# Optimization experiments

Measured on AMD Instinct MI355X. Metric: run time of the kernel, lower is better.

## Reference

```python
import jax, jax.numpy as jnp
import numpy as np

B, S, NODE, DEP, R, L, E = 32, 1024, 256, 64, 50, 16, 128


def setup_inputs() -> dict:
    key = jax.random.key(0)
    k1, k2, k3, k4, k5 = jax.random.split(key, 5)
    context = jax.random.normal(k1, (B, S, NODE), dtype=jnp.float32)
    # torch.rand -> uniform [0,1); one [dep, node+dep] matrix per dependency relation
    dep_W = jax.random.uniform(k2, (R, DEP, NODE + DEP), dtype=jnp.float32)
    heads = jax.random.randint(k3, (B, L, E), 0, S, dtype=jnp.int32)
    tails = jax.random.randint(k4, (B, L, E), 0, S, dtype=jnp.int32)
    rels = jax.random.randint(k5, (B, L, E), 0, R, dtype=jnp.int32)
    return {"context": context, "dep_W": dep_W, "heads": heads, "tails": tails, "rels": rels}


def reference(context, dep_W, heads, tails, rels):
    # context: [B,S,node]; dep_W: [R,dep,node+dep]; heads/tails/rels: [B,L,E]
    B_, S_, node = context.shape
    dep = dep_W.shape[1]
    E_ = heads.shape[2]
    batch_off = jnp.arange(B_, dtype=jnp.int32)[:, None] * S_  # [B,1]

    def layer_step(child, layer):
        h, t, r = layer  # each [B,E]
        # gather per-edge tail features (node feature ++ child state from deeper layers)
        ctx_t = jnp.take_along_axis(context, t[:, :, None], axis=1)  # [B,E,node]
        chd_t = jnp.take_along_axis(child, t[:, :, None], axis=1)    # [B,E,dep]
        feat = jnp.concatenate([ctx_t, chd_t], axis=-1)              # [B,E,node+dep]
        W_e = dep_W[r]                                               # [B,E,dep,node+dep]
        # sum(W * feat, dim=1) == relation-indexed matvec
        msg = jnp.einsum('bekd,bed->bek', W_e, feat)                 # [B,E,dep]
        # scatter-average messages onto head nodes (per batch -> flat index)
        idx = (batch_off + h).reshape(-1)                            # [B*E]
        seg = jax.ops.segment_sum(msg.reshape(-1, dep), idx, num_segments=B_ * S_)
        cnt = jax.ops.segment_sum(jnp.ones((B_ * E_,), msg.dtype), idx, num_segments=B_ * S_)
        avg = seg / jnp.maximum(cnt, 1.0)[:, None]
        child_flat = child.reshape(B_ * S_, dep)
        # heads touched this layer get the averaged message (assignment semantics)
        child_new = jnp.where((cnt > 0)[:, None], avg, child_flat).reshape(B_, S_, dep)
        return child_new, None

    child0 = jnp.zeros((B_, S_, dep), context.dtype)
    layers = (jnp.moveaxis(heads, 1, 0), jnp.moveaxis(tails, 1, 0), jnp.moveaxis(rels, 1, 0))
    child, _ = jax.lax.scan(layer_step, child0, layers)  # layer 0 = deepest layer
    return jnp.concatenate([context, child], axis=-1)    # [B,S,node+dep]
```

## Files before the change

kernel.cpp:

```cpp
#include <hip/hip_runtime.h>

constexpr int B_ = 32;
constexpr int S_ = 1024;
constexpr int NODE_ = 256;
constexpr int DEP_ = 64;
constexpr int R_ = 50;
constexpr int L_ = 16;
constexpr int E_ = 128;
constexpr int FEAT_ = NODE_ + DEP_;
constexpr int NEDGE_ = B_ * E_;
constexpr int BS_ = B_ * S_;
constexpr int CH_ = 16;
constexpr int NCH_ = 320;
constexpr int PREB_ = 512;

constexpr size_t N_CHILD  = (size_t)BS_ * DEP_;
constexpr size_t OFF_A0   = N_CHILD;
constexpr size_t OFF_WT   = N_CHILD * 4;
constexpr size_t N_WT     = (size_t)R_ * FEAT_ * DEP_;
constexpr size_t OFF_SORT = OFF_WT + N_WT;
constexpr size_t N_SORT   = (size_t)L_ * NEDGE_;
constexpr size_t OFF_CHUNK= OFF_SORT + N_SORT;
constexpr size_t N_CHUNK_I= (size_t)L_ * NCH_ * 4;
constexpr size_t OFF_HC   = OFF_CHUNK + N_CHUNK_I;
constexpr size_t N_HC     = (size_t)L_ * BS_;
constexpr size_t OFF_MT   = OFF_HC + N_HC;
constexpr size_t OFF_MH   = OFF_MT + N_SORT;
constexpr size_t OFF_MI   = OFF_MH + N_SORT;
constexpr size_t OFF_CD   = OFF_MI + N_SORT;
constexpr size_t N_CD     = (size_t)L_ * NEDGE_ * DEP_;

__global__ void k_pre(const float* __restrict__ W, const int* __restrict__ rels,
                      const int* __restrict__ heads,
                      float* __restrict__ WT2, int* __restrict__ sorted,
                      int4* __restrict__ chunks, int* __restrict__ hc,
                      float* __restrict__ zero_base) {
  int blk = blockIdx.x, tid = threadIdx.x;
  if (blk < L_) {
    int l = blk;
    __shared__ int hist[R_], startA[R_], rank[R_], cstart[R_];
    __shared__ int ntot;
    if (tid < R_) { hist[tid] = 0; rank[tid] = 0; }
    int* hcl = hc + (size_t)l * BS_;
    for (int i = tid; i < BS_; i += 256) hcl[i] = 0;
    __syncthreads();
    for (int ed = tid; ed < NEDGE_; ed += 256) {
      int b = ed >> 7, e = ed & (E_ - 1);
      atomicAdd(&hist[rels[(b * L_ + l) * E_ + e]], 1);
      atomicAdd(&hcl[b * S_ + heads[(b * L_ + l) * E_ + e]], 1);
    }
    __syncthreads();
    if (tid == 0) {
      int s = 0, cs = 0;
      for (int r = 0; r < R_; ++r) {
        startA[r] = s; s += hist[r];
        cstart[r] = cs; cs += (hist[r] + CH_ - 1) / CH_;
      }
      ntot = cs;
    }
    __syncthreads();
    for (int ed = tid; ed < NEDGE_; ed += 256) {
      int b = ed >> 7, e = ed & (E_ - 1);
      int r = rels[(b * L_ + l) * E_ + e];
      int pos = startA[r] + atomicAdd(&rank[r], 1);
      sorted[l * NEDGE_ + pos] = ed;
    }
    if (tid < R_) {
      int n = hist[tid], st = startA[tid], cs = cstart[tid];
      for (int m = 0; m * CH_ < n; ++m) {
        int c = n - m * CH_; if (c > CH_) c = CH_;
        chunks[l * NCH_ + cs + m] = make_int4(tid, st + m * CH_, c, 0);
      }
    }
    __syncthreads();
    for (int i = ntot + tid; i < NCH_; i += 256)
      chunks[l * NCH_ + i] = make_int4(0, 0, 0, 0);
  } else {
    int gtid = (blk - L_) * 256 + tid;
    const int NT = PREB_ * 256;
    for (int gid = gtid; gid < (int)N_WT; gid += NT) {
      int r = gid / 20480;
      int rem = gid - r * 20480;
      int i4 = rem >> 8;
      int k = (rem >> 2) & 63;
      int c = rem & 3;
      WT2[gid] = W[((size_t)r * DEP_ + k) * FEAT_ + 4 * i4 + c];
    }
    float4* z4 = (float4*)zero_base;
    int nz4 = (int)((N_CHILD * 2) / 4);
    for (int i = gtid; i < nz4; i += NT) z4[i] = make_float4(0.f, 0.f, 0.f, 0.f);
  }
}

__device__ __forceinline__ float dot64(const float4* __restrict__ f4,
                                       const float4* __restrict__ w) {
  float a0 = 0.f, a1 = 0.f, a2 = 0.f, a3 = 0.f;
#pragma unroll
  for (int i = 0; i < 16; ++i) {
    float4 f = f4[i];
    a0 = fmaf(w[i].x, f.x, a0);
    a1 = fmaf(w[i].y, f.y, a1);
    a2 = fmaf(w[i].z, f.z, a2);
    a3 = fmaf(w[i].w, f.w, a3);
  }
  return (a0 + a1) + (a2 + a3);
}

__global__ void __launch_bounds__(256) k_ctx(
    const float* __restrict__ context, const float* __restrict__ WT2,
    const int* __restrict__ heads, const int* __restrict__ tails,
    const int* __restrict__ sorted, const int4* __restrict__ chunks,
    const int* __restrict__ hc, float* __restrict__ ctxdot,
    int* __restrict__ m_trow, int* __restrict__ m_hrow,
    float* __restrict__ m_invc) {
  int cid = blockIdx.x;
  int l = cid / NCH_;
  int4 ck = chunks[cid];
  int r = ck.x, start = ck.y, ccnt = ck.z;
  if (ccnt == 0) return;
  int tid = threadIdx.x, s = tid >> 6, k = tid & 63;

  __shared__ float feat[CH_][NODE_];
  __shared__ float part[4][CH_][DEP_];
  __shared__ int trows[CH_];
  __shared__ float invs[CH_];

  if (tid < ccnt) {
    int pos = l * NEDGE_ + start + tid;
    int ed = sorted[pos];
    int b = ed >> 7, e = ed & (E_ - 1);
    int t = tails[(b * L_ + l) * E_ + e];
    int h = heads[(b * L_ + l) * E_ + e];
    int trow = b * S_ + t, hrow = b * S_ + h;
    int tch = (l > 0) && (hc[(size_t)(l - 1) * BS_ + trow] > 0);
    float invc = 1.0f / (float)hc[(size_t)l * BS_ + hrow];
    m_trow[pos] = trow | (tch ? (int)0x80000000 : 0);
    m_hrow[pos] = hrow;
    m_invc[pos] = invc;
    trows[tid] = trow;
    invs[tid] = invc;
  }
  __syncthreads();

  int tr[CH_];
#pragma unroll
  for (int j = 0; j < CH_; ++j) tr[j] = trows[(j < ccnt) ? j : (ccnt - 1)];

  const float4* Wp = (const float4*)WT2 + ((size_t)r * 80 + s * 16) * 64 + k;
  float4 w[16];
#pragma unroll
  for (int i = 0; i < 16; ++i) w[i] = Wp[(size_t)i * 64];

#pragma unroll
  for (int j = 0; j < CH_; ++j)
    feat[j][tid] = context[(size_t)tr[j] * NODE_ + tid];
  __syncthreads();

  for (int j = 0; j < ccnt; ++j)
    part[s][j][k] = dot64((const float4*)&feat[j][s * 64], w);
  __syncthreads();

  for (int idx = tid; idx < ccnt * DEP_; idx += 256) {
    int j = idx >> 6, k2 = idx & 63;
    ctxdot[(size_t)(l * NEDGE_ + start + j) * DEP_ + k2] =
        (part[0][j][k2] + part[1][j][k2] + part[2][j][k2] + part[3][j][k2]) *
        invs[j];
  }
}

__global__ void __launch_bounds__(256) k_layer(
    const float* __restrict__ WT2, float* __restrict__ child,
    const int4* __restrict__ chunks, const int* __restrict__ m_trow,
    const int* __restrict__ m_hrow, const float* __restrict__ m_invc,
    const float* __restrict__ ctxdot, int l,
    const float* __restrict__ Aprev, float* __restrict__ Acur,
    float* __restrict__ Anext) {
  int tid = threadIdx.x;
  int4 ck = chunks[l * NCH_ + blockIdx.x];
  int r = ck.x, start = ck.y, ccnt = ck.z;
  __shared__ float feat[CH_][DEP_];

  if (ccnt > 0) {
    int wv = tid >> 6, k = tid & 63;

    const float4* Wp = (const float4*)WT2 + ((size_t)r * 80 + 64) * 64 + k;
    float4 w[16];
#pragma unroll
    for (int i = 0; i < 16; ++i) w[i] = Wp[(size_t)i * 64];

    int jj[4], valid[4], tch[4], trow[4], hrow[4];
    float invc[4];
#pragma unroll
    for (int u = 0; u < 4; ++u) {
      int j = wv + 4 * u;
      valid[u] = (j < ccnt);
      jj[u] = valid[u] ? j : (ccnt - 1);
      int pos = l * NEDGE_ + start + jj[u];
      int tr = m_trow[pos];
      tch[u] = (tr < 0);
      trow[u] = tr & 0x7fffffff;
      hrow[u] = m_hrow[pos];
      invc[u] = m_invc[pos];
    }

    float v[4];
#pragma unroll
    for (int u = 0; u < 4; ++u) {
      const float* p = tch[u] ? Aprev : child;
      v[u] = p[(size_t)trow[u] * DEP_ + k];
    }
#pragma unroll
    for (int u = 0; u < 4; ++u) feat[jj[u]][k] = v[u];
    __syncthreads();

#pragma unroll
    for (int u = 0; u < 4; ++u) {
      float d = dot64((const float4*)&feat[jj[u]][0], w);
      int pos = l * NEDGE_ + start + jj[u];
      float contrib = d * invc[u] + ctxdot[(size_t)pos * DEP_ + k];
      if (valid[u]) atomicAdd(&Acur[(size_t)hrow[u] * DEP_ + k], contrib);
    }
  }

  int gtid = blockIdx.x * 256 + tid;
  const int NT = NCH_ * 256;
  if (l > 0) {
    const float4* Ap4 = (const float4*)Aprev;
    float4* ch4 = (float4*)child;
    const int* mh = m_hrow + (size_t)(l - 1) * NEDGE_;
    for (int idx = gtid; idx < NEDGE_ * 16; idx += NT) {
      int pos = idx >> 4, c4 = idx & 15;
      int hrow = mh[pos];
      ch4[(size_t)hrow * 16 + c4] = Ap4[(size_t)hrow * 16 + c4];
    }
  }
  if (l + 1 < L_) {
    float4* An4 = (float4*)Anext;
    const int* mh = m_hrow + (size_t)(l + 1) * NEDGE_;
    float4 z = make_float4(0.f, 0.f, 0.f, 0.f);
    for (int idx = gtid; idx < NEDGE_ * 16; idx += NT) {
      int pos = idx >> 4, c4 = idx & 15;
      An4[(size_t)mh[pos] * 16 + c4] = z;
    }
  }
}

__global__ void k_out(const float4* __restrict__ ctx4,
                      const float4* __restrict__ chd4,
                      const float4* __restrict__ A04,
                      const int* __restrict__ hc15,
                      float4* __restrict__ out4) {
  constexpr int TOT4 = B_ * S_ * (FEAT_ / 4);
  int i = blockIdx.x * blockDim.x + threadIdx.x;
  if (i >= TOT4) return;
  int row = i / 80;
  int c4 = i - row * 80;
  float4 v;
  if (c4 < 64) {
    v = ctx4[(size_t)row * 64 + c4];
  } else {
    int k4 = c4 - 64;
    v = (hc15[row] > 0) ? A04[(size_t)row * 16 + k4]
                        : chd4[(size_t)row * 16 + k4];
  }
  out4[i] = v;
}

extern "C" void kernel_launch(void* const* d_in, const int* in_sizes, int n_in,
                              void* d_out, int out_size, void* d_ws, size_t ws_size,
                              hipStream_t stream) {
  const float* context = (const float*)d_in[0];
  const float* dep_W   = (const float*)d_in[1];
  const int*   heads   = (const int*)d_in[2];
  const int*   tails   = (const int*)d_in[3];
  const int*   rels    = (const int*)d_in[4];
  float* out = (float*)d_out;

  float* ws = (float*)d_ws;
  float* child  = ws;
  float* A[3] = { ws + OFF_A0, ws + OFF_A0 + N_CHILD, ws + OFF_A0 + 2 * N_CHILD };
  float* WT2    = ws + OFF_WT;
  int*   sorted = (int*)(ws + OFF_SORT);
  int4*  chunks = (int4*)(ws + OFF_CHUNK);
  int*   hc     = (int*)(ws + OFF_HC);
  int*   m_trow = (int*)(ws + OFF_MT);
  int*   m_hrow = (int*)(ws + OFF_MH);
  float* m_invc = ws + OFF_MI;
  float* ctxdot = ws + OFF_CD;

  k_pre<<<L_ + PREB_, 256, 0, stream>>>(dep_W, rels, heads, WT2, sorted,
                                        chunks, hc, child);

  k_ctx<<<L_ * NCH_, 256, 0, stream>>>(context, WT2, heads, tails, sorted,
                                       chunks, hc, ctxdot, m_trow, m_hrow,
                                       m_invc);

  for (int l = 0; l < L_; ++l) {
    float* Acur  = A[l % 3];
    float* Aprev = A[(l + 2) % 3];
    float* Anext = A[(l + 1) % 3];
    k_layer<<<NCH_, 256, 0, stream>>>(WT2, child, chunks, m_trow, m_hrow,
                                      m_invc, ctxdot, l, Aprev, Acur, Anext);
  }

  constexpr int TOT4 = B_ * S_ * (FEAT_ / 4);
  k_out<<<(TOT4 + 255) / 256, 256, 0, stream>>>(
      (const float4*)context, (const float4*)child, (const float4*)A[0],
      hc + (size_t)(L_ - 1) * BS_, (float4*)out);
}
```

Baseline: 310.9 us.

## Regroup context matvec edges by relation across layers into 64-edge register-tiled chunks

```diff
diff --git a/kernel.cpp b/kernel.cpp
--- a/kernel.cpp
+++ b/kernel.cpp
@@ -13,6 +13,8 @@
 constexpr int CH_ = 16;
 constexpr int NCH_ = 320;
 constexpr int PREB_ = 512;
+constexpr int GCH_ = 64;
+constexpr int NGC_ = 1088;
 
 constexpr size_t N_CHILD  = (size_t)BS_ * DEP_;
 constexpr size_t OFF_A0   = N_CHILD;
@@ -29,6 +31,8 @@
 constexpr size_t OFF_MI   = OFF_MH + N_SORT;
 constexpr size_t OFF_CD   = OFF_MI + N_SORT;
 constexpr size_t N_CD     = (size_t)L_ * NEDGE_ * DEP_;
+constexpr size_t OFF_GIDX = OFF_CD + N_CD;
+constexpr size_t OFF_GCH  = OFF_GIDX + N_SORT;
 
 __global__ void k_pre(const float* __restrict__ W, const int* __restrict__ rels,
                       const int* __restrict__ heads,
@@ -92,6 +96,48 @@
   }
 }
 
+__global__ void k_gbin(const int4* __restrict__ chunks, int* __restrict__ gidx,
+                       int4* __restrict__ gchunks) {
+  __shared__ int ghist[R_], goff[R_], grank[R_], gcs[R_];
+  int tid = threadIdx.x;
+  if (tid < R_) { ghist[tid] = 0; grank[tid] = 0; }
+  __syncthreads();
+  for (int i = tid; i < L_ * NCH_; i += 1024) {
+    int4 ck = chunks[i];
+    if (ck.z > 0) atomicAdd(&ghist[ck.x], ck.z);
+  }
+  __syncthreads();
+  if (tid == 0) {
+    int s = 0, cs = 0;
+    for (int r = 0; r < R_; ++r) {
+      goff[r] = s; s += ghist[r];
+      gcs[r] = cs; cs += (ghist[r] + GCH_ - 1) / GCH_;
+    }
+  }
+  __syncthreads();
+  for (int i = tid; i < L_ * NCH_; i += 1024) {
+    int4 ck = chunks[i];
+    if (ck.z > 0) {
+      int l = i / NCH_;
+      int base = atomicAdd(&grank[ck.x], ck.z);
+      for (int m = 0; m < ck.z; ++m)
+        gidx[goff[ck.x] + base + m] = l * NEDGE_ + ck.y + m;
+    }
+  }
+  __syncthreads();
+  if (tid < R_) {
+    int n = ghist[tid], go = goff[tid], cs = gcs[tid];
+    for (int m = 0; m * GCH_ < n; ++m) {
+      int c = n - m * GCH_; if (c > GCH_) c = GCH_;
+      gchunks[cs + m] = make_int4(tid, go + m * GCH_, c, 0);
+    }
+  }
+  __syncthreads();
+  int ntot = gcs[R_ - 1] + (ghist[R_ - 1] + GCH_ - 1) / GCH_;
+  for (int i = ntot + tid; i < NGC_; i += 1024)
+    gchunks[i] = make_int4(0, 0, 0, 0);
+}
+
 __device__ __forceinline__ float dot64(const float4* __restrict__ f4,
                                        const float4* __restrict__ w) {
   float a0 = 0.f, a1 = 0.f, a2 = 0.f, a3 = 0.f;
@@ -106,65 +152,104 @@
   return (a0 + a1) + (a2 + a3);
 }
 
-__global__ void __launch_bounds__(256) k_ctx(
+__device__ __forceinline__ void fma4(float& a, float4 w, float4 f) {
+  a = fmaf(w.x, f.x, a);
+  a = fmaf(w.y, f.y, a);
+  a = fmaf(w.z, f.z, a);
+  a = fmaf(w.w, f.w, a);
+}
+
+__global__ void __launch_bounds__(256, 4) k_ctx2(
     const float* __restrict__ context, const float* __restrict__ WT2,
     const int* __restrict__ heads, const int* __restrict__ tails,
-    const int* __restrict__ sorted, const int4* __restrict__ chunks,
-    const int* __restrict__ hc, float* __restrict__ ctxdot,
-    int* __restrict__ m_trow, int* __restrict__ m_hrow,
-    float* __restrict__ m_invc) {
-  int cid = blockIdx.x;
-  int l = cid / NCH_;
-  int4 ck = chunks[cid];
-  int r = ck.x, start = ck.y, ccnt = ck.z;
-  if (ccnt == 0) return;
-  int tid = threadIdx.x, s = tid >> 6, k = tid & 63;
-
-  __shared__ float feat[CH_][NODE_];
-  __shared__ float part[4][CH_][DEP_];
-  __shared__ int trows[CH_];
-  __shared__ float invs[CH_];
-
-  if (tid < ccnt) {
-    int pos = l * NEDGE_ + start + tid;
+    const int* __restrict__ sorted, const int4* __restrict__ gchunks,
+    const int* __restrict__ gidx, const int* __restrict__ hc,
+    float* __restrict__ ctxdot, int* __restrict__ m_trow,
+    int* __restrict__ m_hrow, float* __restrict__ m_invc) {
+  int4 ck = gchunks[blockIdx.x];
+  int r = ck.x, gstart = ck.y, gcnt = ck.z;
+  if (gcnt == 0) return;
+  int tid = threadIdx.x;
+  int tk = tid & 15, tj = tid >> 4;
+
+  __shared__ float4 Wn_s[16 * 64];
+  __shared__ __align__(16) float F_s[GCH_][68];
+  __shared__ int   trow_s[GCH_];
+  __shared__ float invc_s[GCH_];
+  __shared__ int   pos_s[GCH_];
+
+  if (tid < GCH_) {
+    int jj = (tid < gcnt) ? tid : (gcnt - 1);
+    int pos = gidx[gstart + jj];
+    int l = pos >> 12;
     int ed = sorted[pos];
     int b = ed >> 7, e = ed & (E_ - 1);
     int t = tails[(b * L_ + l) * E_ + e];
     int h = heads[(b * L_ + l) * E_ + e];
     int trow = b * S_ + t, hrow = b * S_ + h;
-    int tch = (l > 0) && (hc[(size_t)(l - 1) * BS_ + trow] > 0);
     float invc = 1.0f / (float)hc[(size_t)l * BS_ + hrow];
-    m_trow[pos] = trow | (tch ? (int)0x80000000 : 0);
-    m_hrow[pos] = hrow;
-    m_invc[pos] = invc;
-    trows[tid] = trow;
-    invs[tid] = invc;
-  }
-  __syncthreads();
-
-  int tr[CH_];
-#pragma unroll
-  for (int j = 0; j < CH_; ++j) tr[j] = trows[(j < ccnt) ? j : (ccnt - 1)];
-
-  const float4* Wp = (const float4*)WT2 + ((size_t)r * 80 + s * 16) * 64 + k;
-  float4 w[16];
-#pragma unroll
-  for (int i = 0; i < 16; ++i) w[i] = Wp[(size_t)i * 64];
-
-#pragma unroll
-  for (int j = 0; j < CH_; ++j)
-    feat[j][tid] = context[(size_t)tr[j] * NODE_ + tid];
-  __syncthreads();
-
-  for (int j = 0; j < ccnt; ++j)
-    part[s][j][k] = dot64((const float4*)&feat[j][s * 64], w);
-  __syncthreads();
-
-  for (int idx = tid; idx < ccnt * DEP_; idx += 256) {
-    int j = idx >> 6, k2 = idx & 63;
-    ctxdot[(size_t)(l * NEDGE_ + start + j) * DEP_ + k2] =
-        (part[0][j][k2] + part[1][j][k2] + part[2][j][k2] + part[3][j][k2]) *
-        invs[j];
+    trow_s[tid] = trow;
+    invc_s[tid] = invc;
+    pos_s[tid] = pos;
+    if (tid < gcnt) {
+      int tch = (l > 0) && (hc[(size_t)(l - 1) * BS_ + trow] > 0);
+      m_trow[pos] = trow | (tch ? (int)0x80000000 : 0);
+      m_hrow[pos] = hrow;
+      m_invc[pos] = invc;
+    }
+  }
+  __syncthreads();
+
+  float acc[4][4] = {};
+  const float4* ctx4 = (const float4*)context;
+  const float4* W4 = (const float4*)WT2 + (size_t)r * 80 * 64;
+
+  int jrow = tid >> 2;
+  int c0 = tid & 3;
+  int trowj = trow_s[jrow];
+
+  for (int dp = 0; dp < 4; ++dp) {
+#pragma unroll
+    for (int rep = 0; rep < 4; ++rep) {
+      int idx = tid + 256 * rep;
+      Wn_s[idx] = W4[1024 * dp + idx];
+    }
+#pragma unroll
+    for (int rep = 0; rep < 4; ++rep) {
+      int c4 = c0 + 4 * rep;
+      float4 v = ctx4[(size_t)trowj * 64 + dp * 16 + c4];
+      *(float4*)&F_s[jrow][4 * c4] = v;
+    }
+    __syncthreads();
+
+#pragma unroll
+    for (int i4 = 0; i4 < 16; ++i4) {
+      float4 wv[4], fv[4];
+#pragma unroll
+      for (int a = 0; a < 4; ++a) wv[a] = Wn_s[i4 * 64 + 4 * tk + a];
+#pragma unroll
+      for (int bb = 0; bb < 4; ++bb)
+        fv[bb] = *(const float4*)&F_s[4 * tj + bb][4 * i4];
+#pragma unroll
+      for (int a = 0; a < 4; ++a)
+#pragma unroll
+        for (int bb = 0; bb < 4; ++bb) fma4(acc[a][bb], wv[a], fv[bb]);
+    }
+    __syncthreads();
+  }
+
+#pragma unroll
+  for (int bb = 0; bb < 4; ++bb) {
+    int j = 4 * tj + bb;
+    if (j < gcnt) {
+      float iv = invc_s[j];
+      float4 o;
+      o.x = acc[0][bb] * iv;
+      o.y = acc[1][bb] * iv;
+      o.z = acc[2][bb] * iv;
+      o.w = acc[3][bb] * iv;
+      ((float4*)ctxdot)[(size_t)pos_s[j] * 16 + tk] = o;
+    }
   }
 }
 
@@ -287,13 +372,17 @@
   int*   m_hrow = (int*)(ws + OFF_MH);
   float* m_invc = ws + OFF_MI;
   float* ctxdot = ws + OFF_CD;
+  int*   gidx   = (int*)(ws + OFF_GIDX);
+  int4*  gchunks= (int4*)(ws + OFF_GCH);
 
   k_pre<<<L_ + PREB_, 256, 0, stream>>>(dep_W, rels, heads, WT2, sorted,
                                         chunks, hc, child);
 
-  k_ctx<<<L_ * NCH_, 256, 0, stream>>>(context, WT2, heads, tails, sorted,
-                                       chunks, hc, ctxdot, m_trow, m_hrow,
-                                       m_invc);
+  k_gbin<<<1, 1024, 0, stream>>>(chunks, gidx, gchunks);
+
+  k_ctx2<<<NGC_, 256, 0, stream>>>(context, WT2, heads, tails, sorted,
+                                   gchunks, gidx, hc, ctxdot, m_trow, m_hrow,
+                                   m_invc);
 
   for (int l = 0; l < L_; ++l) {
     float* Acur  = A[l % 3];
```

Result: slower. 318.0 us (+2.3%).
